# Performance work log

Measured on AMD Instinct MI355X. Metric: run time of the kernel, lower is better.

The kernel has to match this reference:

```python
import jax, jax.numpy as jnp
import numpy as np

B, C, T = 8, 512, 8192
NQ, CBS, CBD = 9, 1024, 8
EPS = 1e-12  # F.normalize eps


def setup_inputs() -> dict:
    key = jax.random.key(0)
    ks = jax.random.split(key, 12)
    n = lambda i, shape, s: jax.random.normal(ks[i], shape, jnp.float32) * s
    return {
        "z": n(0, (B, C, T), 1.0),
        "down_w": n(1, (2, C, C, 2), 0.02),   # [layer, out, in, k] (torch Conv1d layout)
        "down_b": n(2, (2, C), 0.01),
        "up_w": n(3, (2, C, C, 2), 0.02),     # [layer, in, out, k] (torch ConvTranspose1d layout)
        "up_b": n(4, (2, C), 0.01),
        "in_v": n(5, (NQ, CBD, C), 0.05),     # weight_norm direction of in_proj 1x1 conv
        "in_g": 1.0 + n(6, (NQ, CBD), 0.02),  # weight_norm magnitude
        "in_b": n(7, (NQ, CBD), 0.01),
        "out_v": n(8, (NQ, C, CBD), 0.05),
        "out_g": 1.0 + n(9, (NQ, C), 0.02),
        "out_b": n(10, (NQ, C), 0.01),
        "codebooks": n(11, (NQ, CBS, CBD), 1.0),
    }


def _wn(g, v):
    # weight_norm (dim=0): per-output-row rescale
    return g[:, None] * v / jnp.linalg.norm(v, axis=1, keepdims=True)


def _l2norm(x):
    return x / jnp.maximum(jnp.linalg.norm(x, axis=-1, keepdims=True), EPS)


def _forward(z, down_w, down_b, up_w, up_b, in_v, in_g, in_b, out_v, out_g, out_b, codebooks):
    # --- downsample: two Conv1d(k=2, s=2) ---
    x = z
    for l in range(2):
        b, c, t = x.shape
        xr = x.reshape(b, c, t // 2, 2)
        x = jnp.einsum('bitk,oik->bot', xr, down_w[l]) + down_b[l][None, :, None]

    residual = x
    z_q = jnp.zeros_like(x)
    commit_loss = jnp.float32(0.0)
    cb_loss = jnp.float32(0.0)
    codes = []
    for i in range(NQ):
        # in_proj 1x1 conv (weight-normed)
        w_in = _wn(in_g[i], in_v[i])                 # [CBD, C]
        z_e = jnp.einsum('bdt,cd->bct', residual, w_in) + in_b[i][None, :, None]  # [B, CBD, T']
        # decode_latents: L2-normalize + squared-euclid via matmul + argmax
        bt = z_e.shape[0] * z_e.shape[2]
        enc = z_e.transpose(0, 2, 1).reshape(bt, CBD)
        enc_n = _l2norm(enc)
        cbk = codebooks[i]
        cb_n = _l2norm(cbk)
        dist = ((enc_n ** 2).sum(1, keepdims=True)
                - 2.0 * enc_n @ cb_n.T
                + (cb_n ** 2).sum(1)[None, :])        # [B*T', CBS]
        idx = jnp.argmax(-dist, axis=1).reshape(z_e.shape[0], -1)  # [B, T']
        z_q_i = cbk[idx].transpose(0, 2, 1)           # [B, CBD, T'] (un-normalized codebook rows)
        # losses (eval: mask all-true -> per-batch mean over (1,2) then batch mean == global mean)
        commit_loss = commit_loss + ((z_e - jax.lax.stop_gradient(z_q_i)) ** 2).mean()
        cb_loss = cb_loss + ((z_q_i - jax.lax.stop_gradient(z_e)) ** 2).mean()
        # straight-through + out_proj 1x1 conv (weight-normed)
        z_st = z_e + jax.lax.stop_gradient(z_q_i - z_e)
        w_out = _wn(out_g[i], out_v[i])               # [C, CBD]
        z_q_out = jnp.einsum('bct,dc->bdt', z_st, w_out) + out_b[i][None, :, None]
        z_q = z_q + z_q_out
        residual = residual - z_q_out
        codes.append(idx)
    codes = jnp.stack(codes, axis=1)                  # [B, NQ, T']

    x = z_q
    for l in range(2):
        b, c, t = x.shape
        x = jnp.einsum('bit,iok->botk', x, up_w[l]).reshape(b, C, t * 2) + up_b[l][None, :, None]
    return x, codes, commit_loss, cb_loss


def reference(z, down_w, down_b, up_w, up_b, in_v, in_g, in_b, out_v, out_g, out_b, codebooks):
    return _forward(z, down_w, down_b, up_w, up_b, in_v, in_g, in_b, out_v, out_g, out_b, codebooks)
```

## Files before the change

### kernel.cpp

```cpp
#include <hip/hip_runtime.h>
#include <math.h>


using u16 = unsigned short;
typedef __attribute__((ext_vector_type(8))) short bf16x8;
typedef __attribute__((ext_vector_type(8))) u16 su16x8;
typedef __attribute__((ext_vector_type(4))) float f32x4;

constexpr int NQ = 9, CBS = 1024, CBD = 8;
constexpr int TQ = 2048;
constexpr int NTOK = 16384;
constexpr int APS = 1048576;
#define EPSN 1e-12f

constexpr size_t OFF_X2    = 0;
constexpr size_t OFF_E0T   = 8388608;
constexpr size_t OFF_Q     = 9568256;
constexpr size_t OFF_WD    = 10747904;
constexpr size_t OFF_WDP   = 11796480;
constexpr size_t OFF_WEFF  = 13369344;
constexpr size_t OFF_WX    = 14417920;
constexpr size_t OFF_WINN  = 14581760;
constexpr size_t OFF_WOUTS = 14618624;
constexpr size_t OFF_CBS   = 14659584;
constexpr size_t OFF_PT    = 14678016;
constexpr size_t OFF_BEFF  = 14680356;
constexpr size_t OFF_BSUM  = 14680428;
constexpr size_t OFF_BD    = 14680940;
constexpr size_t OFF_BUP   = 14681452;
constexpr size_t OFF_LOSS  = 14682476;

__global__ void prep_small1(const float* __restrict__ in_v, const float* __restrict__ in_g,
                            const float* __restrict__ out_v, const float* __restrict__ out_g,
                            const float* __restrict__ out_b, const float* __restrict__ codebooks,
                            const float* __restrict__ down_w, const float* __restrict__ down_b,
                            const float* __restrict__ up_w, const float* __restrict__ up_b,
                            float* __restrict__ ws) {
  int bid = blockIdx.x, tid = threadIdx.x;
  int wid4 = tid >> 6, lane = tid & 63;
  if (bid < 18) {
    int wid = bid * 4 + wid4;
    if (wid < 72) {
      const float* v = in_v + (size_t)wid * 512;
      float ss = 0.f;
      for (int c = lane; c < 512; c += 64) ss += v[c] * v[c];
      #pragma unroll
      for (int o = 32; o; o >>= 1) ss += __shfl_xor(ss, o);
      float sc = in_g[wid] / sqrtf(ss);
      float* dst = ws + OFF_WINN + (size_t)wid * 512;
      for (int c = lane; c < 512; c += 64) dst[c] = v[c] * sc;
    }
  } else if (bid < 36) {
    int r = (bid - 18) * 256 + tid;
    if (r < 4608) {
      int i = r >> 9, c = r & 511;
      const float* v = out_v + (size_t)r * 8;
      float ss = 0.f;
      #pragma unroll
      for (int d = 0; d < 8; d++) ss += v[d] * v[d];
      float sc = out_g[r] / sqrtf(ss);
      float* dst = ws + OFF_WOUTS + (size_t)c * 80 + i * 8;
      #pragma unroll
      for (int d = 0; d < 8; d++) dst[d] = v[d] * sc;
    }
  } else if (bid < 72) {
    int r = (bid - 36) * 256 + tid;
    if (r < 9216) {
      int i = r >> 10, j = r & 1023;
      const float* v = codebooks + (size_t)r * 8;
      float ss = 0.f;
      #pragma unroll
      for (int d = 0; d < 8; d++) ss += v[d] * v[d];
      float nm = fmaxf(sqrtf(ss), EPSN);
      float nsq = 0.f;
      #pragma unroll
      for (int d = 0; d < 8; d++) { float cn = v[d] / nm; nsq += cn * cn; }
      ws[OFF_CBS + ((size_t)i * 2 + 0) * 1024 + j] = 2.0f / nm;
      ws[OFF_CBS + ((size_t)i * 2 + 1) * 1024 + j] = nsq;
    }
  } else if (bid < 74) {
    int c = (bid - 72) * 256 + tid;
    if (c < 512) {
      float s = 0.f;
      #pragma unroll
      for (int j = 0; j < 9; j++) s += out_b[j * 512 + c];
      ws[OFF_BSUM + c] = s;
      ws[OFF_WOUTS + (size_t)c * 80 + 72] = s;
      #pragma unroll
      for (int d = 73; d < 80; d++) ws[OFF_WOUTS + (size_t)c * 80 + d] = 0.f;
    }
  } else if (bid < 202) {
    int o = (bid - 74) * 4 + wid4;
    float s = 0.f;
    for (int m = lane; m < 512; m += 64) {
      float w0 = down_w[524288 + (size_t)o * 1024 + m * 2];
      float w1 = down_w[524288 + (size_t)o * 1024 + m * 2 + 1];
      s += (w0 + w1) * down_b[m];
    }
    #pragma unroll
    for (int off = 32; off; off >>= 1) s += __shfl_xor(s, off);
    if (lane == 0) ws[OFF_BD + o] = s + down_b[512 + o];
  } else {
    int gw = (bid - 202) * 4 + wid4;
    int c = gw >> 1, j2 = gw & 1;
    float s = 0.f;
    for (int m = lane; m < 512; m += 64)
      s += up_w[524288 + (size_t)m * 1024 + c * 2 + j2] * up_b[m];
    #pragma unroll
    for (int off = 32; off; off >>= 1) s += __shfl_xor(s, off);
    if (lane == 0) ws[OFF_BUP + gw] = s + up_b[512 + c];
  }
}

__global__ void prep2(const float* __restrict__ in_b, const float* __restrict__ out_b,
                      float* __restrict__ ws) {
  int gw = blockIdx.x * 4 + (threadIdx.x >> 6), lane = threadIdx.x & 63;
  const float* WinN = ws + OFF_WINN;
  const float* WoutS = ws + OFF_WOUTS;
  if (gw < 2304) {
    int tri = gw >> 6, dd = gw & 63;
    int ip = 1;
    while (tri >= ip * (ip + 1) / 2) ip++;
    int i = tri - ip * (ip - 1) / 2;
    int d = dd >> 3, dp = dd & 7;
    const float* a = WinN + (size_t)(ip * 8 + d) * 512;
    float s = 0.f;
    for (int c = lane; c < 512; c += 64) s += a[c] * WoutS[(size_t)c * 80 + i * 8 + dp];
    #pragma unroll
    for (int o = 32; o; o >>= 1) s += __shfl_xor(s, o);
    if (lane == 0) ws[OFF_PT + (size_t)tri * 65 + dd] = s;
  } else if (gw < 2376) {
    int r = gw - 2304;
    int i = r >> 3;
    const float* a = WinN + (size_t)r * 512;
    float s = 0.f;
    for (int c = lane; c < 512; c += 64) {
      float ob = 0.f;
      for (int j = 0; j < i; j++) ob += out_b[j * 512 + c];
      s += a[c] * ob;
    }
    #pragma unroll
    for (int o = 32; o; o >>= 1) s += __shfl_xor(s, o);
    if (lane == 0) ws[OFF_BEFF + r] = in_b[r] - s;
  }
}

template <int WHICH>
__global__ __launch_bounds__(256) void smallmm(const float* __restrict__ src,
                                               float* __restrict__ outp) {
  __shared__ float As[32][68];
  __shared__ float Bs[32][68];
  const int tid = threadIdx.x;
  const int tx = tid & 15, ty = tid >> 4;
  const int b0 = blockIdx.x * 64, a0 = blockIdx.y * 64, j = blockIdx.z;
  const int jh = j >> 1, jl = j & 1;
  float acc[4][4];
  #pragma unroll
  for (int i = 0; i < 4; i++)
    #pragma unroll
    for (int k = 0; k < 4; k++) acc[i][k] = 0.f;

  for (int k0 = 0; k0 < 512; k0 += 32) {
    #pragma unroll
    for (int rep = 0; rep < 8; rep++) {
      int f = tid + rep * 256;
      int aa = f >> 5, mm = f & 31;
      size_t ai;
      if constexpr (WHICH == 0) ai = 524288 + (size_t)(a0 + aa) * 1024 + (k0 + mm) * 2 + jh;
      else                      ai = 524288 + (size_t)(k0 + mm) * 1024 + (a0 + aa) * 2 + jl;
      As[mm][aa] = src[ai];
      int mm2 = f >> 6, bb = f & 63;
      size_t bi;
      if constexpr (WHICH == 0) bi = (size_t)(k0 + mm2) * 1024 + (b0 + bb) * 2 + jl;
      else                      bi = (size_t)(b0 + bb) * 1024 + (k0 + mm2) * 2 + jh;
      Bs[mm2][bb] = src[bi];
    }
    __syncthreads();
    #pragma unroll
    for (int kk = 0; kk < 32; kk++) {
      float av[4], bv[4];
      #pragma unroll
      for (int i = 0; i < 4; i++) av[i] = As[kk][ty * 4 + i];
      #pragma unroll
      for (int i = 0; i < 4; i++) bv[i] = Bs[kk][tx * 4 + i];
      #pragma unroll
      for (int i = 0; i < 4; i++)
        #pragma unroll
        for (int k = 0; k < 4; k++) acc[i][k] = fmaf(av[i], bv[k], acc[i][k]);
    }
    __syncthreads();
  }
  #pragma unroll
  for (int i = 0; i < 4; i++) {
    int a = a0 + ty * 4 + i;
    #pragma unroll
    for (int k = 0; k < 4; k++) {
      int b = b0 + tx * 4 + k;
      if constexpr (WHICH == 0) outp[(size_t)a * 2048 + b * 4 + j] = acc[i][k];
      else                      outp[((size_t)a * 4 + j) * 512 + b] = acc[i][k];
    }
  }
}

__global__ void prep_wdsplit(const float* __restrict__ wd, u16* __restrict__ wdp) {
  int idx = blockIdx.x * 256 + threadIdx.x;
  float v = wd[idx];
  unsigned u = __float_as_uint(v);
  wdp[idx] = (u16)(u >> 16);
  float r = v - __uint_as_float(u & 0xFFFF0000u);
  unsigned ur = __float_as_uint(r);
  wdp[APS + idx] = (u16)(ur >> 16);
  float r2 = r - __uint_as_float(ur & 0xFFFF0000u);
  wdp[2 * APS + idx] = (u16)(__float_as_uint(r2) >> 16);
}

__global__ __launch_bounds__(256) void prep_wx(const float* __restrict__ weff,
                                               const float* __restrict__ wouts,
                                               float* __restrict__ wx) {
  __shared__ float Wes[16][512];
  __shared__ float WSs[64][80];
  const int tid = threadIdx.x;
  const int m0 = blockIdx.x * 16;
  #pragma unroll
  for (int rep = 0; rep < 32; rep++) {
    int f = tid + rep * 256;
    Wes[f >> 9][f & 511] = weff[(size_t)(m0 + (f >> 9)) * 512 + (f & 511)];
  }
  const int rowq = tid >> 4, rq = tid & 15;
  float accs[5] = {0.f, 0.f, 0.f, 0.f, 0.f};
  for (int k0 = 0; k0 < 512; k0 += 64) {
    __syncthreads();
    #pragma unroll
    for (int rep = 0; rep < 20; rep++) {
      int f = tid + rep * 256;
      int kk = f / 80, col = f % 80;
      WSs[kk][col] = wouts[(size_t)(k0 + kk) * 80 + col];
    }
    __syncthreads();
    #pragma unroll 4
    for (int kk = 0; kk < 64; kk++) {
      float we = Wes[rowq][k0 + kk];
      #pragma unroll
      for (int s = 0; s < 5; s++) accs[s] = fmaf(we, WSs[kk][rq + 16 * s], accs[s]);
    }
  }
  #pragma unroll
  for (int s = 0; s < 5; s++) {
    int r = rq + 16 * s;
    if (r < 73) wx[(size_t)(m0 + rowq) * 80 + r] = accs[s];
  }
  if (tid < 112) {
    int row = tid / 7, col = 73 + tid % 7;
    wx[(size_t)(m0 + row) * 80 + col] = 0.f;
  }
}

__global__ __launch_bounds__(256) void gemm_down(const u16* __restrict__ Ap,
                                                 const float* __restrict__ z,
                                                 const float* __restrict__ bias,
                                                 float* __restrict__ Out) {
  constexpr int NS = 3, K = 2048;
  __shared__ u16 Bp[2][NS][128][32];
  const int tid = threadIdx.x;
  const int w = tid >> 6, l = tid & 63;
  const int g = l >> 4, li = l & 15;
  const int wr = w >> 1, wc = w & 1;
  const int n0 = blockIdx.x * 128, m0 = blockIdx.y * 128;
  const int nn = tid & 127, kw = tid >> 7;
  const int bb = n0 >> 11;
  const int tb = (n0 & 2047) + nn;

  f32x4 acc[4][4];
  #pragma unroll
  for (int a = 0; a < 4; a++)
    #pragma unroll
    for (int b = 0; b < 4; b++) acc[a][b] = (f32x4){0.f, 0.f, 0.f, 0.f};

  float pvA[16], pvB[16];
  bf16x8 afrA[4][NS], afrB[4][NS];
  const u16* arow = Ap + (size_t)(m0 + wr * 64 + li) * K + g * 8;

#define LOADB(PV, K0)                                                           \
  {                                                                             \
    int c0_ = ((K0) >> 2) + kw * 4;                                             \
    _Pragma("unroll")                                                           \
    for (int cc_ = 0; cc_ < 4; ++cc_)                                           \
      *(float4*)&PV[4 * cc_] =                                                  \
          *(const float4*)(z + ((size_t)(bb * 512 + c0_ + cc_) << 13) + 4 * tb);\
  }

#define LOADA(DST, K0)                                                          \
  {                                                                             \
    _Pragma("unroll")                                                           \
    for (int fm_ = 0; fm_ < 4; ++fm_)                                           \
      _Pragma("unroll")                                                         \
      for (int p_ = 0; p_ < NS; ++p_)                                           \
        DST[fm_][p_] = *(const bf16x8*)(arow + (size_t)p_ * APS +               \
                                        (size_t)fm_ * 16 * K + (K0));           \
  }

  const int sw = (nn >> 1) & 3;
  const int c0 = ((2 * kw) ^ sw) << 3, c1 = ((2 * kw + 1) ^ sw) << 3;

#define STAGE(BUF, PV)                                                          \
  {                                                                             \
    su16x8 pa_[NS], pb_[NS];                                                    \
    _Pragma("unroll")                                                           \
    for (int j_ = 0; j_ < 8; ++j_) {                                            \
      {                                                                         \
        float v_ = PV[j_];                                                      \
        unsigned u_ = __float_as_uint(v_);                                      \
        pa_[0][j_] = (u16)(u_ >> 16);                                           \
        float r_ = v_ - __uint_as_float(u_ & 0xFFFF0000u);                      \
        unsigned ur_ = __float_as_uint(r_);                                     \
        pa_[1][j_] = (u16)(ur_ >> 16);                                          \
        float r2_ = r_ - __uint_as_float(ur_ & 0xFFFF0000u);                    \
        pa_[2][j_] = (u16)(__float_as_uint(r2_) >> 16);                         \
      }                                                                         \
      {                                                                         \
        float v_ = PV[8 + j_];                                                  \
        unsigned u_ = __float_as_uint(v_);                                      \
        pb_[0][j_] = (u16)(u_ >> 16);                                           \
        float r_ = v_ - __uint_as_float(u_ & 0xFFFF0000u);                      \
        unsigned ur_ = __float_as_uint(r_);                                     \
        pb_[1][j_] = (u16)(ur_ >> 16);                                          \
        float r2_ = r_ - __uint_as_float(ur_ & 0xFFFF0000u);                    \
        pb_[2][j_] = (u16)(__float_as_uint(r2_) >> 16);                         \
      }                                                                         \
    }                                                                           \
    _Pragma("unroll")                                                           \
    for (int p_ = 0; p_ < NS; ++p_) {                                           \
      *(su16x8*)&Bp[BUF][p_][nn][c0] = pa_[p_];                                 \
      *(su16x8*)&Bp[BUF][p_][nn][c1] = pb_[p_];                                 \
    }                                                                           \
  }

#define COMPUTE(BUF, AFR)                                                       \
  {                                                                             \
    _Pragma("unroll")                                                           \
    for (int fn_ = 0; fn_ < 4; ++fn_) {                                         \
      int row_ = wc * 64 + fn_ * 16 + li;                                       \
      int cs_ = ((g ^ ((row_ >> 1) & 3)) << 3);                                 \
      bf16x8 bfr_[NS];                                                          \
      _Pragma("unroll")                                                         \
      for (int q_ = 0; q_ < NS; ++q_)                                           \
        bfr_[q_] = *(const bf16x8*)&Bp[BUF][q_][row_][cs_];                     \
      _Pragma("unroll")                                                         \
      for (int fm_ = 0; fm_ < 4; ++fm_) {                                       \
        f32x4 a_ = acc[fm_][fn_];                                               \
        a_ = __builtin_amdgcn_mfma_f32_16x16x32_bf16(AFR[fm_][2], bfr_[0], a_, 0, 0, 0); \
        a_ = __builtin_amdgcn_mfma_f32_16x16x32_bf16(AFR[fm_][1], bfr_[1], a_, 0, 0, 0); \
        a_ = __builtin_amdgcn_mfma_f32_16x16x32_bf16(AFR[fm_][0], bfr_[2], a_, 0, 0, 0); \
        a_ = __builtin_amdgcn_mfma_f32_16x16x32_bf16(AFR[fm_][1], bfr_[0], a_, 0, 0, 0); \
        a_ = __builtin_amdgcn_mfma_f32_16x16x32_bf16(AFR[fm_][0], bfr_[1], a_, 0, 0, 0); \
        a_ = __builtin_amdgcn_mfma_f32_16x16x32_bf16(AFR[fm_][0], bfr_[0], a_, 0, 0, 0); \
        acc[fm_][fn_] = a_;                                                     \
      }                                                                         \
    }                                                                           \
  }

  LOADB(pvA, 0)
  LOADB(pvB, 32)
  STAGE(0, pvA)
  LOADB(pvA, 64)
  LOADA(afrA, 0)
  __syncthreads();

  for (int k0 = 0; k0 < K; k0 += 64) {
    STAGE(1, pvB)
    if (k0 + 96 < K) { LOADB(pvB, k0 + 96) }
    LOADA(afrB, k0 + 32)
    COMPUTE(0, afrA)
    __syncthreads();
    if (k0 + 64 < K) { STAGE(0, pvA) }
    if (k0 + 128 < K) { LOADB(pvA, k0 + 128) }
    if (k0 + 64 < K) { LOADA(afrA, k0 + 64) }
    COMPUTE(1, afrB)
    __syncthreads();
  }
#undef LOADB
#undef LOADA
#undef STAGE
#undef COMPUTE

  const int mb = m0 + wr * 64 + g * 4;
  const int nb = n0 + wc * 64 + li;
  #pragma unroll
  for (int fn = 0; fn < 4; ++fn) {
    int n = nb + fn * 16;
    int b = n >> 11, t = n & 2047;
    #pragma unroll
    for (int fm = 0; fm < 4; ++fm)
      #pragma unroll
      for (int r = 0; r < 4; ++r) {
        int o = mb + fm * 16 + r;
        Out[((size_t)((b << 9) + o)) * 2048 + t] = acc[fm][fn][r] + bias[o];
      }
  }
}

__global__ __launch_bounds__(256) void gemm_e0f(const float* __restrict__ A,
                                                const float* __restrict__ Bsrc,
                                                float* __restrict__ e0t) {
  constexpr int M = 72, K = 512, Tt = 2048;
  __shared__ float As[16][132];
  __shared__ float Bs[16][68];
  int tid = threadIdx.x;
  int tx = tid & 7, ty = tid >> 3;
  int n0 = blockIdx.x * 64;
  int b = n0 / Tt, t0 = n0 % Tt;
  float acc[4][8];
  #pragma unroll
  for (int i = 0; i < 4; i++)
    #pragma unroll
    for (int j = 0; j < 8; j++) acc[i][j] = 0.f;

  for (int k0 = 0; k0 < K; k0 += 16) {
    #pragma unroll
    for (int rep = 0; rep < 2; rep++) {
      int f = tid + rep * 256;
      int row = f >> 2, c4 = (f & 3) << 2;
      int m = row, k = k0 + c4;
      float4 v = make_float4(0.f, 0.f, 0.f, 0.f);
      if (m < M) v = *(const float4*)(A + (size_t)m * K + k);
      As[c4 + 0][row] = v.x; As[c4 + 1][row] = v.y;
      As[c4 + 2][row] = v.z; As[c4 + 3][row] = v.w;
    }
    {
      int kk = tid >> 4, n4 = (tid & 15) << 2;
      float4 v = *(const float4*)(Bsrc + ((size_t)(b * K + k0 + kk)) * Tt + t0 + n4);
      *(float4*)&Bs[kk][n4] = v;
    }
    __syncthreads();
    #pragma unroll
    for (int kk = 0; kk < 16; kk++) {
      float a[4], bb[8];
      #pragma unroll
      for (int i = 0; i < 4; i++) a[i] = As[kk][ty * 4 + i];
      *(float4*)&bb[0] = *(float4*)&Bs[kk][tx * 8];
      *(float4*)&bb[4] = *(float4*)&Bs[kk][tx * 8 + 4];
      #pragma unroll
      for (int i = 0; i < 4; i++)
        #pragma unroll
        for (int j = 0; j < 8; j++) acc[i][j] = fmaf(a[i], bb[j], acc[i][j]);
    }
    __syncthreads();
  }
  #pragma unroll
  for (int j = 0; j < 8; j++) {
    int n = n0 + tx * 8 + j;
    #pragma unroll
    for (int i = 0; i < 4; i++) {
      int m = ty * 4 + i;
      if (m < M) e0t[(size_t)n * M + m] = acc[i][j];
    }
  }
}

__global__ __launch_bounds__(256) void xfin(const float* __restrict__ wx,
                                            const float* __restrict__ Q,
                                            const float* __restrict__ bup,
                                            float* __restrict__ xout) {
  __shared__ float Wxs[128][80];
  __shared__ float Qs[128][80];
  const int tid = threadIdx.x;
  const int n0 = blockIdx.x * 128, m0 = blockIdx.y * 128;
  #pragma unroll
  for (int rep = 0; rep < 10; rep++) {
    int f = tid + rep * 256;
    *(float4*)&Wxs[0][f * 4] = *(const float4*)(wx + (size_t)m0 * 80 + f * 4);
  }
  {
    int nn = tid & 127, r0 = tid >> 7;
    for (int r = r0; r < 72; r += 2)
      Qs[nn][r] = Q[(size_t)r * 16384 + n0 + nn];
  }
  __syncthreads();

  const int txn = tid & 15, tym = tid >> 4;
  float acc[8][8];
  #pragma unroll
  for (int i = 0; i < 8; i++)
    #pragma unroll
    for (int j = 0; j < 8; j++) acc[i][j] = 0.f;

  #pragma unroll 2
  for (int r4 = 0; r4 < 18; r4++) {
    float4 wv[8], qv[8];
    #pragma unroll
    for (int i = 0; i < 8; i++) wv[i] = *(const float4*)&Wxs[tym * 8 + i][r4 * 4];
    #pragma unroll
    for (int j = 0; j < 8; j++) qv[j] = *(const float4*)&Qs[txn * 8 + j][r4 * 4];
    #pragma unroll
    for (int i = 0; i < 8; i++)
      #pragma unroll
      for (int j = 0; j < 8; j++) {
        acc[i][j] = fmaf(wv[i].x, qv[j].x, acc[i][j]);
        acc[i][j] = fmaf(wv[i].y, qv[j].y, acc[i][j]);
        acc[i][j] = fmaf(wv[i].z, qv[j].z, acc[i][j]);
        acc[i][j] = fmaf(wv[i].w, qv[j].w, acc[i][j]);
      }
  }

  float bxv[8];
  #pragma unroll
  for (int mi = 0; mi < 8; mi++) {
    int mp = m0 + tym * 8 + mi;
    bxv[mi] = Wxs[tym * 8 + mi][72] + bup[(mp >> 2) * 2 + (mp & 1)];
  }
  #pragma unroll
  for (int cg = 0; cg < 2; cg++) {
    int mp0 = m0 + tym * 8 + cg * 4;
    int c = mp0 >> 2;
    #pragma unroll
    for (int j = 0; j < 8; j++) {
      int n = n0 + txn * 8 + j;
      int b = n >> 11, t = n & 2047;
      float4 sv = make_float4(acc[cg * 4 + 0][j] + bxv[cg * 4 + 0],
                              acc[cg * 4 + 1][j] + bxv[cg * 4 + 1],
                              acc[cg * 4 + 2][j] + bxv[cg * 4 + 2],
                              acc[cg * 4 + 3][j] + bxv[cg * 4 + 3]);
      *(float4*)&xout[((size_t)((b << 9) + c)) * 8192 + 4 * t] = sv;
    }
  }
}

__global__ __launch_bounds__(256) void rvq_kernel(const float* __restrict__ codebooks,
                                                  const float* __restrict__ e0t,
                                                  const float* __restrict__ cbsW,
                                                  const float* __restrict__ ptW,
                                                  const float* __restrict__ beffW,
                                                  float* __restrict__ Qout,
                                                  float* __restrict__ codesOut,
                                                  float* __restrict__ lossPart) {
  __shared__ float cbv[8][1024];
  __shared__ float cbs2[2][1024];
  __shared__ float Pt[36 * 65];
  __shared__ float est[16][72];
  __shared__ float lred[4];
  int tid = threadIdx.x, wid = tid >> 6, lane = tid & 63;
  int nb0 = blockIdx.x * 16;
  for (int idx = tid; idx < 2340; idx += 256) Pt[idx] = ptW[idx];
  for (int idx = tid; idx < 16 * 72; idx += 256)
    est[idx / 72][idx % 72] = e0t[(size_t)nb0 * 72 + idx] + beffW[idx % 72];
  float lossLocal = 0.f;

  for (int i = 0; i < NQ; i++) {
    __syncthreads();
    const float* cbg = codebooks + (size_t)i * CBS * CBD;
    for (int lin = tid; lin < 2048; lin += 256) {
      int j = lin >> 1, half = (lin & 1) << 2;
      float4 v = *(const float4*)(cbg + (size_t)j * 8 + half);
      cbv[half + 0][j] = v.x; cbv[half + 1][j] = v.y;
      cbv[half + 2][j] = v.z; cbv[half + 3][j] = v.w;
    }
    for (int lin = tid; lin < 1024; lin += 256) {
      cbs2[0][lin] = cbsW[((size_t)i * 2 + 0) * 1024 + lin];
      cbs2[1][lin] = cbsW[((size_t)i * 2 + 1) * 1024 + lin];
    }
    __syncthreads();

    float ze[4][8], en[4][8];
    #pragma unroll
    for (int w = 0; w < 4; w++) {
      int tokl = wid * 4 + w;
      float ss = 0.f;
      #pragma unroll
      for (int d = 0; d < 8; d++) { float v = est[tokl][i * 8 + d]; ze[w][d] = v; ss += v * v; }
      float inv = 1.0f / fmaxf(sqrtf(ss), EPSN);
      #pragma unroll
      for (int d = 0; d < 8; d++) en[w][d] = ze[w][d] * inv;
    }
    float best[4]; int bidx[4];
    #pragma unroll
    for (int w = 0; w < 4; w++) { best[w] = -INFINITY; bidx[w] = 0; }
    #pragma unroll 4
    for (int r = 0; r < 16; r++) {
      int j = lane + (r << 6);
      float c0 = cbv[0][j], c1 = cbv[1][j], c2 = cbv[2][j], c3 = cbv[3][j];
      float c4 = cbv[4][j], c5 = cbv[5][j], c6 = cbv[6][j], c7 = cbv[7][j];
      float ti = cbs2[0][j], ns = cbs2[1][j];
      #pragma unroll
      for (int w = 0; w < 4; w++) {
        float dt = en[w][0] * c0;
        dt = fmaf(en[w][1], c1, dt); dt = fmaf(en[w][2], c2, dt);
        dt = fmaf(en[w][3], c3, dt); dt = fmaf(en[w][4], c4, dt);
        dt = fmaf(en[w][5], c5, dt); dt = fmaf(en[w][6], c6, dt);
        dt = fmaf(en[w][7], c7, dt);
        float s = fmaf(dt, ti, -ns);
        if (s > best[w]) { best[w] = s; bidx[w] = j; }
      }
    }
    #pragma unroll
    for (int w = 0; w < 4; w++) {
      #pragma unroll
      for (int off = 32; off; off >>= 1) {
        float so = __shfl_xor(best[w], off);
        int jo = __shfl_xor(bidx[w], off);
        if (so > best[w] || (so == best[w] && jo < bidx[w])) { best[w] = so; bidx[w] = jo; }
      }
    }
    int d = lane & 7;
    #pragma unroll
    for (int w = 0; w < 4; w++) {
      int jstar = bidx[w];
      int tokl = wid * 4 + w;
      int n = nb0 + tokl;
      float qd = cbv[d][jstar];
      float diff = ze[w][d] - qd;
      float sq = diff * diff;
      sq += __shfl_xor(sq, 1); sq += __shfl_xor(sq, 2); sq += __shfl_xor(sq, 4);
      if (lane == 0) lossLocal += sq;
      if (lane < 8) Qout[(size_t)(i * 8 + lane) * NTOK + n] = qd;
      if (lane == 0) codesOut[(size_t)((n >> 11) * NQ + i) * TQ + (n & (TQ - 1))] = (float)jstar;
      if (i < NQ - 1) {
        int f = lane >> 3, d2 = lane & 7;
        int ip = i + 1 + f;
        if (ip < NQ) {
          int tri = (ip * (ip - 1)) / 2 + i;
          const float* prow = &Pt[tri * 65 + d2 * 8];
          float s = 0.f;
          #pragma unroll
          for (int dp = 0; dp < 8; dp++) s = fmaf(prow[dp], cbv[dp][jstar], s);
          est[tokl][ip * 8 + d2] -= s;
        }
      }
    }
  }
  if (lane == 0) lred[wid] = lossLocal;
  __syncthreads();
  if (tid == 0) {
    float s = ((lred[0] + lred[1]) + lred[2]) + lred[3];
    lossPart[blockIdx.x] = s;
  }
}

__global__ void loss_fin(const float* __restrict__ lossPart, float* __restrict__ out) {
  __shared__ float s[256];
  int tid = threadIdx.x;
  float v = 0.f;
  for (int r = 0; r < 4; r++) v += lossPart[tid + r * 256];
  s[tid] = v;
  __syncthreads();
  for (int w = 128; w; w >>= 1) {
    if (tid < w) s[tid] += s[tid + w];
    __syncthreads();
  }
  if (tid == 0) {
    float total = s[0] / 131072.0f;
    out[0] = total;
    out[1] = total;
  }
}

extern "C" void kernel_launch(void* const* d_in, const int* in_sizes, int n_in,
                              void* d_out, int out_size, void* d_ws, size_t ws_size,
                              hipStream_t stream) {
  const float* z      = (const float*)d_in[0];
  const float* down_w = (const float*)d_in[1];
  const float* down_b = (const float*)d_in[2];
  const float* up_w   = (const float*)d_in[3];
  const float* up_b   = (const float*)d_in[4];
  const float* in_v   = (const float*)d_in[5];
  const float* in_g   = (const float*)d_in[6];
  const float* in_b   = (const float*)d_in[7];
  const float* out_v  = (const float*)d_in[8];
  const float* out_g  = (const float*)d_in[9];
  const float* out_b  = (const float*)d_in[10];
  const float* codebooks = (const float*)d_in[11];
  float* ws = (float*)d_ws;
  float* xout = (float*)d_out;
  float* codesOut = xout + (size_t)8 * 512 * 8192;
  float* lossOut = codesOut + (size_t)8 * NQ * TQ;

  hipLaunchKernelGGL(prep_small1, dim3(458), dim3(256), 0, stream,
                     in_v, in_g, out_v, out_g, out_b, codebooks,
                     down_w, down_b, up_w, up_b, ws);
  hipLaunchKernelGGL(prep2, dim3(594), dim3(256), 0, stream, in_b, out_b, ws);
  hipLaunchKernelGGL((smallmm<0>), dim3(8, 8, 4), dim3(256), 0, stream, down_w, ws + OFF_WD);
  hipLaunchKernelGGL((smallmm<1>), dim3(8, 8, 4), dim3(256), 0, stream, up_w, ws + OFF_WEFF);
  hipLaunchKernelGGL(prep_wdsplit, dim3(4096), dim3(256), 0, stream,
                     ws + OFF_WD, (u16*)(ws + OFF_WDP));
  hipLaunchKernelGGL(prep_wx, dim3(128), dim3(256), 0, stream,
                     ws + OFF_WEFF, ws + OFF_WOUTS, ws + OFF_WX);
  hipLaunchKernelGGL(gemm_down, dim3(128, 4), dim3(256), 0, stream,
                     (const u16*)(ws + OFF_WDP), z, ws + OFF_BD, ws + OFF_X2);
  hipLaunchKernelGGL(gemm_e0f, dim3(256), dim3(256), 0, stream,
                     ws + OFF_WINN, ws + OFF_X2, ws + OFF_E0T);
  hipLaunchKernelGGL(rvq_kernel, dim3(1024), dim3(256), 0, stream,
                     codebooks, ws + OFF_E0T, ws + OFF_CBS, ws + OFF_PT, ws + OFF_BEFF,
                     ws + OFF_Q, codesOut, ws + OFF_LOSS);
  hipLaunchKernelGGL(xfin, dim3(128, 16), dim3(256), 0, stream,
                     ws + OFF_WX, ws + OFF_Q, ws + OFF_BUP, xout);
  hipLaunchKernelGGL(loss_fin, dim3(1), dim3(256), 0, stream, ws + OFF_LOSS, lossOut);
}
```

Before: 813.6 us.

## Merge prep kernels, stream A fragments in GEMM, token-major Q layout

Merges the two small weight GEMMs into one launch, and the bf16 split with prep_wx into another. prep_small1's up-bias part now uses one thread per output instead of one wave. In gemm_down, A fragments are loaded from global memory just before use instead of being prefetched into registers a stage ahead. The Q buffer is stored token-major (80 floats per token) so xfin can load it with float4 copies, and rvq_kernel reads Pt from global memory instead of staging it in shared memory. The aim is fewer launches, less register pressure and coalesced Q loads, at the cost of exposed global-load latency in the GEMM inner loop.

```diff
diff --git a/kernel.cpp b/kernel.cpp
--- a/kernel.cpp
+++ b/kernel.cpp
@@ -16,19 +16,19 @@
 constexpr size_t OFF_X2    = 0;
 constexpr size_t OFF_E0T   = 8388608;
 constexpr size_t OFF_Q     = 9568256;
-constexpr size_t OFF_WD    = 10747904;
-constexpr size_t OFF_WDP   = 11796480;
-constexpr size_t OFF_WEFF  = 13369344;
-constexpr size_t OFF_WX    = 14417920;
-constexpr size_t OFF_WINN  = 14581760;
-constexpr size_t OFF_WOUTS = 14618624;
-constexpr size_t OFF_CBS   = 14659584;
-constexpr size_t OFF_PT    = 14678016;
-constexpr size_t OFF_BEFF  = 14680356;
-constexpr size_t OFF_BSUM  = 14680428;
-constexpr size_t OFF_BD    = 14680940;
-constexpr size_t OFF_BUP   = 14681452;
-constexpr size_t OFF_LOSS  = 14682476;
+constexpr size_t OFF_WD    = 10878976;
+constexpr size_t OFF_WDP   = 11927552;
+constexpr size_t OFF_WEFF  = 13500416;
+constexpr size_t OFF_WX    = 14548992;
+constexpr size_t OFF_WINN  = 14712832;
+constexpr size_t OFF_WOUTS = 14749696;
+constexpr size_t OFF_CBS   = 14790656;
+constexpr size_t OFF_PT    = 14809088;
+constexpr size_t OFF_BEFF  = 14811428;
+constexpr size_t OFF_BSUM  = 14811500;
+constexpr size_t OFF_BD    = 14812012;
+constexpr size_t OFF_BUP   = 14812524;
+constexpr size_t OFF_LOSS  = 14813548;
 
 __global__ void prep_small1(const float* __restrict__ in_v, const float* __restrict__ in_g,
                             const float* __restrict__ out_v, const float* __restrict__ out_g,
@@ -101,14 +101,12 @@
     for (int off = 32; off; off >>= 1) s += __shfl_xor(s, off);
     if (lane == 0) ws[OFF_BD + o] = s + down_b[512 + o];
   } else {
-    int gw = (bid - 202) * 4 + wid4;
+    int gw = (bid - 202) * 256 + tid;
     int c = gw >> 1, j2 = gw & 1;
     float s = 0.f;
-    for (int m = lane; m < 512; m += 64)
+    for (int m = 0; m < 512; m++)
       s += up_w[524288 + (size_t)m * 1024 + c * 2 + j2] * up_b[m];
-    #pragma unroll
-    for (int off = 32; off; off >>= 1) s += __shfl_xor(s, off);
-    if (lane == 0) ws[OFF_BUP + gw] = s + up_b[512 + c];
+    ws[OFF_BUP + gw] = s + up_b[512 + c];
   }
 }
 
@@ -145,15 +143,18 @@
   }
 }
 
-template <int WHICH>
-__global__ __launch_bounds__(256) void smallmm(const float* __restrict__ src,
-                                               float* __restrict__ outp) {
+__global__ __launch_bounds__(256) void smallmm2(const float* __restrict__ down_w,
+                                                const float* __restrict__ up_w,
+                                                float* __restrict__ wd,
+                                                float* __restrict__ weff) {
   __shared__ float As[32][68];
   __shared__ float Bs[32][68];
   const int tid = threadIdx.x;
   const int tx = tid & 15, ty = tid >> 4;
-  const int b0 = blockIdx.x * 64, a0 = blockIdx.y * 64, j = blockIdx.z;
+  const int b0 = blockIdx.x * 64, a0 = blockIdx.y * 64;
+  const int which = blockIdx.z >> 2, j = blockIdx.z & 3;
   const int jh = j >> 1, jl = j & 1;
+  const float* src = which ? up_w : down_w;
   float acc[4][4];
   #pragma unroll
   for (int i = 0; i < 4; i++)
@@ -165,14 +166,12 @@
     for (int rep = 0; rep < 8; rep++) {
       int f = tid + rep * 256;
       int aa = f >> 5, mm = f & 31;
-      size_t ai;
-      if constexpr (WHICH == 0) ai = 524288 + (size_t)(a0 + aa) * 1024 + (k0 + mm) * 2 + jh;
-      else                      ai = 524288 + (size_t)(k0 + mm) * 1024 + (a0 + aa) * 2 + jl;
+      size_t ai = which ? (524288 + (size_t)(k0 + mm) * 1024 + (a0 + aa) * 2 + jl)
+                        : (524288 + (size_t)(a0 + aa) * 1024 + (k0 + mm) * 2 + jh);
       As[mm][aa] = src[ai];
       int mm2 = f >> 6, bb = f & 63;
-      size_t bi;
-      if constexpr (WHICH == 0) bi = (size_t)(k0 + mm2) * 1024 + (b0 + bb) * 2 + jl;
-      else                      bi = (size_t)(b0 + bb) * 1024 + (k0 + mm2) * 2 + jh;
+      size_t bi = which ? ((size_t)(b0 + bb) * 1024 + (k0 + mm2) * 2 + jh)
+                        : ((size_t)(k0 + mm2) * 1024 + (b0 + bb) * 2 + jl);
       Bs[mm2][bb] = src[bi];
     }
     __syncthreads();
@@ -196,31 +195,33 @@
     #pragma unroll
     for (int k = 0; k < 4; k++) {
       int b = b0 + tx * 4 + k;
-      if constexpr (WHICH == 0) outp[(size_t)a * 2048 + b * 4 + j] = acc[i][k];
-      else                      outp[((size_t)a * 4 + j) * 512 + b] = acc[i][k];
-    }
-  }
-}
-
-__global__ void prep_wdsplit(const float* __restrict__ wd, u16* __restrict__ wdp) {
-  int idx = blockIdx.x * 256 + threadIdx.x;
-  float v = wd[idx];
-  unsigned u = __float_as_uint(v);
-  wdp[idx] = (u16)(u >> 16);
-  float r = v - __uint_as_float(u & 0xFFFF0000u);
-  unsigned ur = __float_as_uint(r);
-  wdp[APS + idx] = (u16)(ur >> 16);
-  float r2 = r - __uint_as_float(ur & 0xFFFF0000u);
-  wdp[2 * APS + idx] = (u16)(__float_as_uint(r2) >> 16);
-}
-
-__global__ __launch_bounds__(256) void prep_wx(const float* __restrict__ weff,
-                                               const float* __restrict__ wouts,
-                                               float* __restrict__ wx) {
+      if (which) weff[((size_t)a * 4 + j) * 512 + b] = acc[i][k];
+      else       wd[(size_t)a * 2048 + b * 4 + j] = acc[i][k];
+    }
+  }
+}
+
+__global__ __launch_bounds__(256) void prep_split_wx(const float* __restrict__ wd,
+                                                     u16* __restrict__ wdp,
+                                                     const float* __restrict__ weff,
+                                                     const float* __restrict__ wouts,
+                                                     float* __restrict__ wx) {
+  const int tid = threadIdx.x;
+  if (blockIdx.x < 4096) {
+    int idx = blockIdx.x * 256 + tid;
+    float v = wd[idx];
+    unsigned u = __float_as_uint(v);
+    wdp[idx] = (u16)(u >> 16);
+    float r = v - __uint_as_float(u & 0xFFFF0000u);
+    unsigned ur = __float_as_uint(r);
+    wdp[APS + idx] = (u16)(ur >> 16);
+    float r2 = r - __uint_as_float(ur & 0xFFFF0000u);
+    wdp[2 * APS + idx] = (u16)(__float_as_uint(r2) >> 16);
+    return;
+  }
   __shared__ float Wes[16][512];
   __shared__ float WSs[64][80];
-  const int tid = threadIdx.x;
-  const int m0 = blockIdx.x * 16;
+  const int m0 = (blockIdx.x - 4096) * 16;
   #pragma unroll
   for (int rep = 0; rep < 32; rep++) {
     int f = tid + rep * 256;
@@ -277,8 +278,6 @@
     for (int b = 0; b < 4; b++) acc[a][b] = (f32x4){0.f, 0.f, 0.f, 0.f};
 
   float pvA[16], pvB[16];
-  bf16x8 afrA[4][NS], afrB[4][NS];
-  const u16* arow = Ap + (size_t)(m0 + wr * 64 + li) * K + g * 8;
 
 #define LOADB(PV, K0)                                                           \
   {                                                                             \
@@ -287,16 +286,6 @@
     for (int cc_ = 0; cc_ < 4; ++cc_)                                           \
       *(float4*)&PV[4 * cc_] =                                                  \
           *(const float4*)(z + ((size_t)(bb * 512 + c0_ + cc_) << 13) + 4 * tb);\
-  }
-
-#define LOADA(DST, K0)                                                          \
-  {                                                                             \
-    _Pragma("unroll")                                                           \
-    for (int fm_ = 0; fm_ < 4; ++fm_)                                           \
-      _Pragma("unroll")                                                         \
-      for (int p_ = 0; p_ < NS; ++p_)                                           \
-        DST[fm_][p_] = *(const bf16x8*)(arow + (size_t)p_ * APS +               \
-                                        (size_t)fm_ * 16 * K + (K0));           \
   }
 
   const int sw = (nn >> 1) & 3;
@@ -335,25 +324,33 @@
     }                                                                           \
   }
 
-#define COMPUTE(BUF, AFR)                                                       \
+#define COMPUTE(BUF, K0)                                                        \
   {                                                                             \
+    bf16x8 bfr_[4][NS];                                                         \
     _Pragma("unroll")                                                           \
     for (int fn_ = 0; fn_ < 4; ++fn_) {                                         \
       int row_ = wc * 64 + fn_ * 16 + li;                                       \
       int cs_ = ((g ^ ((row_ >> 1) & 3)) << 3);                                 \
-      bf16x8 bfr_[NS];                                                          \
       _Pragma("unroll")                                                         \
       for (int q_ = 0; q_ < NS; ++q_)                                           \
-        bfr_[q_] = *(const bf16x8*)&Bp[BUF][q_][row_][cs_];                     \
+        bfr_[fn_][q_] = *(const bf16x8*)&Bp[BUF][q_][row_][cs_];                \
+    }                                                                           \
+    const u16* arow_ = Ap + (size_t)(m0 + wr * 64 + li) * K + (K0) + g * 8;     \
+    _Pragma("unroll")                                                           \
+    for (int fm_ = 0; fm_ < 4; ++fm_) {                                         \
+      bf16x8 afr_[NS];                                                          \
       _Pragma("unroll")                                                         \
-      for (int fm_ = 0; fm_ < 4; ++fm_) {                                       \
+      for (int p_ = 0; p_ < NS; ++p_)                                           \
+        afr_[p_] = *(const bf16x8*)(arow_ + (size_t)p_ * APS + (size_t)fm_ * 16 * K); \
+      _Pragma("unroll")                                                         \
+      for (int fn_ = 0; fn_ < 4; ++fn_) {                                       \
         f32x4 a_ = acc[fm_][fn_];                                               \
-        a_ = __builtin_amdgcn_mfma_f32_16x16x32_bf16(AFR[fm_][2], bfr_[0], a_, 0, 0, 0); \
-        a_ = __builtin_amdgcn_mfma_f32_16x16x32_bf16(AFR[fm_][1], bfr_[1], a_, 0, 0, 0); \
-        a_ = __builtin_amdgcn_mfma_f32_16x16x32_bf16(AFR[fm_][0], bfr_[2], a_, 0, 0, 0); \
-        a_ = __builtin_amdgcn_mfma_f32_16x16x32_bf16(AFR[fm_][1], bfr_[0], a_, 0, 0, 0); \
-        a_ = __builtin_amdgcn_mfma_f32_16x16x32_bf16(AFR[fm_][0], bfr_[1], a_, 0, 0, 0); \
-        a_ = __builtin_amdgcn_mfma_f32_16x16x32_bf16(AFR[fm_][0], bfr_[0], a_, 0, 0, 0); \
+        a_ = __builtin_amdgcn_mfma_f32_16x16x32_bf16(afr_[2], bfr_[fn_][0], a_, 0, 0, 0); \
+        a_ = __builtin_amdgcn_mfma_f32_16x16x32_bf16(afr_[1], bfr_[fn_][1], a_, 0, 0, 0); \
+        a_ = __builtin_amdgcn_mfma_f32_16x16x32_bf16(afr_[0], bfr_[fn_][2], a_, 0, 0, 0); \
+        a_ = __builtin_amdgcn_mfma_f32_16x16x32_bf16(afr_[1], bfr_[fn_][0], a_, 0, 0, 0); \
+        a_ = __builtin_amdgcn_mfma_f32_16x16x32_bf16(afr_[0], bfr_[fn_][1], a_, 0, 0, 0); \
+        a_ = __builtin_amdgcn_mfma_f32_16x16x32_bf16(afr_[0], bfr_[fn_][0], a_, 0, 0, 0); \
         acc[fm_][fn_] = a_;                                                     \
       }                                                                         \
     }                                                                           \
@@ -363,23 +360,19 @@
   LOADB(pvB, 32)
   STAGE(0, pvA)
   LOADB(pvA, 64)
-  LOADA(afrA, 0)
   __syncthreads();
 
   for (int k0 = 0; k0 < K; k0 += 64) {
     STAGE(1, pvB)
     if (k0 + 96 < K) { LOADB(pvB, k0 + 96) }
-    LOADA(afrB, k0 + 32)
-    COMPUTE(0, afrA)
+    COMPUTE(0, k0)
     __syncthreads();
     if (k0 + 64 < K) { STAGE(0, pvA) }
     if (k0 + 128 < K) { LOADB(pvA, k0 + 128) }
-    if (k0 + 64 < K) { LOADA(afrA, k0 + 64) }
-    COMPUTE(1, afrB)
+    COMPUTE(1, k0 + 32)
     __syncthreads();
   }
 #undef LOADB
-#undef LOADA
 #undef STAGE
 #undef COMPUTE
 
@@ -469,11 +462,7 @@
   for (int rep = 0; rep < 10; rep++) {
     int f = tid + rep * 256;
     *(float4*)&Wxs[0][f * 4] = *(const float4*)(wx + (size_t)m0 * 80 + f * 4);
-  }
-  {
-    int nn = tid & 127, r0 = tid >> 7;
-    for (int r = r0; r < 72; r += 2)
-      Qs[nn][r] = Q[(size_t)r * 16384 + n0 + nn];
+    *(float4*)&Qs[0][f * 4] = *(const float4*)(Q + (size_t)n0 * 80 + f * 4);
   }
   __syncthreads();
 
@@ -535,12 +524,10 @@
                                                   float* __restrict__ lossPart) {
   __shared__ float cbv[8][1024];
   __shared__ float cbs2[2][1024];
-  __shared__ float Pt[36 * 65];
   __shared__ float est[16][72];
   __shared__ float lred[4];
   int tid = threadIdx.x, wid = tid >> 6, lane = tid & 63;
   int nb0 = blockIdx.x * 16;
-  for (int idx = tid; idx < 2340; idx += 256) Pt[idx] = ptW[idx];
   for (int idx = tid; idx < 16 * 72; idx += 256)
     est[idx / 72][idx % 72] = e0t[(size_t)nb0 * 72 + idx] + beffW[idx % 72];
   float lossLocal = 0.f;
@@ -611,14 +598,14 @@
       float sq = diff * diff;
       sq += __shfl_xor(sq, 1); sq += __shfl_xor(sq, 2); sq += __shfl_xor(sq, 4);
       if (lane == 0) lossLocal += sq;
-      if (lane < 8) Qout[(size_t)(i * 8 + lane) * NTOK + n] = qd;
+      if (lane < 8) Qout[(size_t)n * 80 + i * 8 + lane] = qd;
       if (lane == 0) codesOut[(size_t)((n >> 11) * NQ + i) * TQ + (n & (TQ - 1))] = (float)jstar;
       if (i < NQ - 1) {
         int f = lane >> 3, d2 = lane & 7;
         int ip = i + 1 + f;
         if (ip < NQ) {
           int tri = (ip * (ip - 1)) / 2 + i;
-          const float* prow = &Pt[tri * 65 + d2 * 8];
+          const float* prow = ptW + (size_t)tri * 65 + d2 * 8;
           float s = 0.f;
           #pragma unroll
           for (int dp = 0; dp < 8; dp++) s = fmaf(prow[dp], cbv[dp][jstar], s);
@@ -673,15 +660,14 @@
   float* codesOut = xout + (size_t)8 * 512 * 8192;
   float* lossOut = codesOut + (size_t)8 * NQ * TQ;
 
-  hipLaunchKernelGGL(prep_small1, dim3(458), dim3(256), 0, stream,
+  hipLaunchKernelGGL(prep_small1, dim3(206), dim3(256), 0, stream,
                      in_v, in_g, out_v, out_g, out_b, codebooks,
                      down_w, down_b, up_w, up_b, ws);
   hipLaunchKernelGGL(prep2, dim3(594), dim3(256), 0, stream, in_b, out_b, ws);
-  hipLaunchKernelGGL((smallmm<0>), dim3(8, 8, 4), dim3(256), 0, stream, down_w, ws + OFF_WD);
-  hipLaunchKernelGGL((smallmm<1>), dim3(8, 8, 4), dim3(256), 0, stream, up_w, ws + OFF_WEFF);
-  hipLaunchKernelGGL(prep_wdsplit, dim3(4096), dim3(256), 0, stream,
-                     ws + OFF_WD, (u16*)(ws + OFF_WDP));
-  hipLaunchKernelGGL(prep_wx, dim3(128), dim3(256), 0, stream,
+  hipLaunchKernelGGL(smallmm2, dim3(8, 8, 8), dim3(256), 0, stream,
+                     down_w, up_w, ws + OFF_WD, ws + OFF_WEFF);
+  hipLaunchKernelGGL(prep_split_wx, dim3(4224), dim3(256), 0, stream,
+                     ws + OFF_WD, (u16*)(ws + OFF_WDP),
                      ws + OFF_WEFF, ws + OFF_WOUTS, ws + OFF_WX);
   hipLaunchKernelGGL(gemm_down, dim3(128, 4), dim3(256), 0, stream,
                      (const u16*)(ws + OFF_WDP), z, ws + OFF_BD, ws + OFF_X2);
```

Result: faster. 780.4 us (-4.1%).
